# Kernel tuning notes

Hardware: AMD Instinct MI355X
Metric: run time of the kernel (lower is better)

## Reference

```python
import jax, jax.numpy as jnp
import numpy as np

N_NODES = 50000
N_EDGES = 800000
D = 64
B = 64
HL = 128  # lstm hidden
OUT = 32


def setup_inputs() -> dict:
    key = jax.random.key(0)
    ks = jax.random.split(key, 16)
    s = 0.05
    return {
        "x": jax.random.normal(ks[0], (N_NODES, D), jnp.float32),
        "edge_index": jax.random.randint(ks[1], (2, N_EDGES), 0, N_NODES),
        "batch": jnp.sort(jax.random.randint(ks[2], (N_NODES,), 0, B)),
        "w1": jax.random.normal(ks[3], (D, D), jnp.float32) * s,
        "b1": jnp.zeros((D,), jnp.float32),
        "w2": jax.random.normal(ks[4], (D, D), jnp.float32) * s,
        "b2": jnp.zeros((D,), jnp.float32),
        "w3": jax.random.normal(ks[5], (D, D), jnp.float32) * s,
        "b3": jnp.zeros((D,), jnp.float32),
        "w4": jax.random.normal(ks[6], (D, D), jnp.float32) * s,
        "b4": jnp.zeros((D,), jnp.float32),
        "w_ih": jax.random.normal(ks[7], (4 * HL, D), jnp.float32) * s,
        "w_hh": jax.random.normal(ks[8], (4 * HL, HL), jnp.float32) * s,
        "b_ih": jnp.zeros((4 * HL,), jnp.float32),
        "b_hh": jnp.zeros((4 * HL,), jnp.float32),
        "fc_w": jax.random.normal(ks[9], (OUT, HL), jnp.float32) * s,
        "fc_b": jnp.zeros((OUT,), jnp.float32),
        "h0": jax.random.normal(ks[10], (1, B, HL), jnp.float32),
        "c0": jax.random.normal(ks[11], (1, B, HL), jnp.float32),
    }


def _gin(x, edge_index, wA, bA, wB, bB):
    # GINConv with eps=0: MLP(x + sum_{j->i} x_j); scatter-add over edges
    agg = jax.ops.segment_sum(x[edge_index[0]], edge_index[1], num_segments=N_NODES)
    h = x + agg
    h = jax.nn.relu(h @ wA.T + bA)
    return h @ wB.T + bB


def reference(x, edge_index, batch, w1, b1, w2, b2, w3, b3, w4, b4,
              w_ih, w_hh, b_ih, b_hh, fc_w, fc_b, h0, c0):
    h = jax.nn.relu(_gin(x, edge_index, w1, b1, w2, b2))  # dropout = identity (eval)
    h = jax.nn.relu(_gin(h, edge_index, w3, b3, w4, b4))
    # global_mean_pool over graphs
    sums = jax.ops.segment_sum(h, batch, num_segments=B)              # [B, D]
    cnts = jax.ops.segment_sum(jnp.ones((N_NODES,), h.dtype), batch, num_segments=B)
    pooled = sums / jnp.maximum(cnts, 1.0)[:, None]
    # single-step LSTM (PyTorch gate order: i, f, g, o)
    gates = pooled @ w_ih.T + b_ih + h0[0] @ w_hh.T + b_hh            # [B, 4H]
    i, f, g, o = jnp.split(gates, 4, axis=-1)
    c1 = jax.nn.sigmoid(f) * c0[0] + jax.nn.sigmoid(i) * jnp.tanh(g)
    h1 = jax.nn.sigmoid(o) * jnp.tanh(c1)
    logits = h1 @ fc_w.T + fc_b
    probs = jax.nn.softmax(logits, axis=1)
    return probs, h1[None], c1[None]
```

## Files before the change

### kernel.cpp

```cpp
#include <hip/hip_runtime.h>
#include <hip/hip_bf16.h>

#define N_NODES 50000
#define N_EDGES 800000
#define D 64
#define B 64
#define HL 128
#define OUT 32

#define CAP 64
#define STP 72
#define ZROW N_NODES

#define BINS 196
#define EPB 2048
#define LCAP 48
#define BCAP 4608

#define AB 391
#define CB 3125
#define MB 782

typedef __attribute__((ext_vector_type(8))) short          short8;
typedef __attribute__((ext_vector_type(8))) unsigned short ushort8_t;
typedef __attribute__((ext_vector_type(4))) float          floatx4;

__device__ __forceinline__ unsigned short f2bf(float f)
{
    unsigned u = __float_as_uint(f);
    u = (u + 0x7FFFu + ((u >> 16) & 1u)) >> 16;
    return (unsigned short)u;
}
__device__ __forceinline__ float bfLO(unsigned u) { return __uint_as_float(u << 16); }
__device__ __forceinline__ float bfHI(unsigned u) { return __uint_as_float(u & 0xffff0000u); }

__global__ __launch_bounds__(256) void pro_kernel(
    const int*   __restrict__ ei,
    int*         __restrict__ bincnt,
    unsigned*    __restrict__ binbuf,
    const float* __restrict__ x, unsigned short* __restrict__ xb,
    const float* __restrict__ w1, const float* __restrict__ w2,
    const float* __restrict__ w3, const float* __restrict__ w4,
    unsigned short* __restrict__ wb,
    unsigned short* __restrict__ h1,
    float*       __restrict__ psum,
    float*       __restrict__ cnts)
{
    __shared__ int      lcnt[BINS];
    __shared__ int      gbase[BINS];
    __shared__ unsigned lbuf[BINS * LCAP];

    int t = threadIdx.x;

    if (blockIdx.x < AB) {
        if (t < BINS) lcnt[t] = 0;
        __syncthreads();

        int base = blockIdx.x * EPB;
#pragma unroll
        for (int i = 0; i < EPB / 256; ++i) {
            int e = base + i * 256 + t;
            if (e < N_EDGES) {
                int s = ei[e];
                int d = ei[N_EDGES + e];
                int bin = d >> 8;
                unsigned pk = (unsigned)s | ((unsigned)(d & 255) << 16);
                int p = atomicAdd(&lcnt[bin], 1);
                if (p < LCAP) {
                    lbuf[bin * LCAP + p] = pk;
                } else {
                    int q = atomicAdd(&bincnt[bin], 1);
                    if (q < BCAP) binbuf[bin * BCAP + q] = pk;
                }
            }
        }
        __syncthreads();

        if (t < BINS) {
            int m = lcnt[t]; m = (m < LCAP) ? m : LCAP;
            gbase[t] = (m > 0) ? atomicAdd(&bincnt[t], m) : 0;
        }
        __syncthreads();

        int wv = t >> 6, lane = t & 63;
        for (int b = wv; b < BINS; b += 4) {
            int m = lcnt[b]; m = (m < LCAP) ? m : LCAP;
            int gb = gbase[b];
            for (int j = lane; j < m; j += 64)
                if (gb + j < BCAP) binbuf[b * BCAP + gb + j] = lbuf[b * LCAP + j];
        }
    } else if (blockIdx.x < AB + CB) {
        int cb = blockIdx.x - AB;
        int i = cb * 256 + t;
        const float4 v = reinterpret_cast<const float4*>(x)[i];
        ushort4 o;
        o.x = f2bf(v.x); o.y = f2bf(v.y); o.z = f2bf(v.z); o.w = f2bf(v.w);
        reinterpret_cast<ushort4*>(xb)[i] = o;

        if (cb < 64) {
            int j = cb * 256 + t;
            int m = j >> 12, off = j & 4095;
            const float* src = (m == 0) ? w1 : (m == 1) ? w2 : (m == 2) ? w3 : w4;
            wb[j] = f2bf(src[off]);
        }
    } else {
        if (t < D) {
            xb[(size_t)ZROW * D + t] = 0;
            h1[(size_t)ZROW * D + t] = 0;
        }
#pragma unroll
        for (int k = 0; k < 16; ++k)
            psum[t * 16 + k] = 0.0f;
        if (t < B) cnts[t] = 0.0f;
    }
}

__device__ __forceinline__ void build_bucket64(
    const int*      __restrict__ bincnt,
    const unsigned* __restrict__ binbuf,
    unsigned short* lbkt,
    int*            lc,
    int bn0, int t)
{
    {
        ushort8_t fill = {ZROW, ZROW, ZROW, ZROW, ZROW, ZROW, ZROW, ZROW};
        for (int i = t; i < (64 * CAP + 16) / 8; i += 512)
            reinterpret_cast<ushort8_t*>(lbkt)[i] = fill;
    }
    if (t < 64) lc[t] = 0;
    __syncthreads();

    const int bin = bn0 >> 8;
    const int q   = (bn0 >> 6) & 3;
    int m = bincnt[bin]; m = (m < BCAP) ? m : BCAP;
    const unsigned* src = binbuf + bin * BCAP;
    for (int j = t; j < m; j += 512) {
        unsigned pk = src[j];
        int dlow = (pk >> 16) & 255;
        if ((dlow >> 6) == q) {
            int r = dlow & 63;
            int p = atomicAdd(&lc[r], 1);
            if (p < CAP) lbkt[r * CAP + p] = (unsigned short)(pk & 0xFFFFu);
        }
    }
    __syncthreads();
}

__device__ __forceinline__ void gather8_bf16(
    const unsigned short* __restrict__ feat,
    const unsigned short* lbkt,
    const int*            lc,
    unsigned short*       stbase,
    int bn0, int wv, int lane)
{
    const int g = lane >> 4;
    const int c = lane & 15;

#pragma unroll
    for (int b = 0; b < 2; ++b) {
        const int rloc = wv * 8 + b * 4 + g;
        const int node = bn0 + rloc;
        int deg = lc[rloc];
        deg = (deg < CAP) ? deg : CAP;
        int m = (deg + 7) >> 3;
        {
            int t1 = __shfl_xor(m, 16); m = (t1 > m) ? t1 : m;
            int t2 = __shfl_xor(m, 32); m = (t2 > m) ? t2 : m;
        }

        const unsigned short* bkt = lbkt + rloc * CAP;

        uint2 u = *reinterpret_cast<const uint2*>(feat + (size_t)node * D + 4 * c);
        float a0 = bfLO(u.x), a1 = bfHI(u.x);
        float a2 = bfLO(u.y), a3 = bfHI(u.y);

        ushort8_t idx = *reinterpret_cast<const ushort8_t*>(bkt);
        for (int r = 0; r < m; ++r) {
            ushort8_t nxt = *reinterpret_cast<const ushort8_t*>(bkt + (r + 1) * 8);
#pragma unroll
            for (int j = 0; j < 8; ++j) {
                uint2 v = *reinterpret_cast<const uint2*>(
                    feat + (size_t)idx[j] * D + 4 * c);
                a0 += bfLO(v.x); a1 += bfHI(v.x);
                a2 += bfLO(v.y); a3 += bfHI(v.y);
            }
            idx = nxt;
        }

        const int tile = wv >> 1;
        const int row  = (wv & 1) * 8 + b * 4 + g;
        uint2 o;
        o.x = (unsigned)f2bf(a0) | ((unsigned)f2bf(a1) << 16);
        o.y = (unsigned)f2bf(a2) | ((unsigned)f2bf(a3) << 16);
        *reinterpret_cast<uint2*>(stbase + (tile * 16 + row) * STP + 4 * c) = o;
    }
}

__global__ __launch_bounds__(512) void gmlp_kernel(
    const unsigned short* __restrict__ feat,
    const int*            __restrict__ bincnt,
    const unsigned*       __restrict__ binbuf,
    const unsigned short* __restrict__ wAb,
    const float*          __restrict__ bA,
    const unsigned short* __restrict__ wBb,
    const float*          __restrict__ bB,
    unsigned short*       __restrict__ outp)
{
    __shared__ int lc[64];
    __shared__ __align__(16) unsigned short lbkt[64 * CAP + 16];
    __shared__ __align__(16) unsigned short st[4][16 * STP];

    const int t    = threadIdx.x;
    const int wv   = t >> 6;
    const int lane = t & 63;
    const int quad = lane >> 4;
    const int col  = lane & 15;

    const int bn0 = blockIdx.x * 64;

    build_bucket64(bincnt, binbuf, lbkt, lc, bn0, t);

    if (bn0 + wv * 8 < N_NODES)
        gather8_bf16(feat, lbkt, lc, &st[0][0], bn0, wv, lane);
    __syncthreads();

    if (wv >= 4) return;
    const int n0 = bn0 + wv * 16;
    if (n0 >= N_NODES) return;

    float bAl[4], bBl[4];
#pragma unroll
    for (int tt = 0; tt < 4; ++tt) {
        bAl[tt] = bA[tt * 16 + col];
        bBl[tt] = bB[tt * 16 + col];
    }

    short8 WA[4][2], WB[4][2];
#pragma unroll
    for (int tt = 0; tt < 4; ++tt)
#pragma unroll
        for (int k = 0; k < 2; ++k) {
            WA[tt][k] = *reinterpret_cast<const short8*>(
                wAb + (tt * 16 + col) * D + k * 32 + quad * 8);
            WB[tt][k] = *reinterpret_cast<const short8*>(
                wBb + (tt * 16 + col) * D + k * 32 + quad * 8);
        }

    unsigned short* stw = &st[wv][0];

    short8 A0 = *reinterpret_cast<const short8*>(stw + col * STP + 0 * 32 + quad * 8);
    short8 A1 = *reinterpret_cast<const short8*>(stw + col * STP + 1 * 32 + quad * 8);

#pragma unroll
    for (int tt = 0; tt < 4; ++tt) {
        floatx4 c = {0.0f, 0.0f, 0.0f, 0.0f};
        c = __builtin_amdgcn_mfma_f32_16x16x32_bf16(A0, WA[tt][0], c, 0, 0, 0);
        c = __builtin_amdgcn_mfma_f32_16x16x32_bf16(A1, WA[tt][1], c, 0, 0, 0);
#pragma unroll
        for (int r = 0; r < 4; ++r) {
            float v = fmaxf(c[r] + bAl[tt], 0.0f);
            stw[(quad * 4 + r) * STP + tt * 16 + col] = f2bf(v);
        }
    }

    short8 T0 = *reinterpret_cast<const short8*>(stw + col * STP + 0 * 32 + quad * 8);
    short8 T1 = *reinterpret_cast<const short8*>(stw + col * STP + 1 * 32 + quad * 8);

#pragma unroll
    for (int tt = 0; tt < 4; ++tt) {
        floatx4 c = {0.0f, 0.0f, 0.0f, 0.0f};
        c = __builtin_amdgcn_mfma_f32_16x16x32_bf16(T0, WB[tt][0], c, 0, 0, 0);
        c = __builtin_amdgcn_mfma_f32_16x16x32_bf16(T1, WB[tt][1], c, 0, 0, 0);
#pragma unroll
        for (int r = 0; r < 4; ++r) {
            float v = fmaxf(c[r] + bBl[tt], 0.0f);
            outp[(size_t)(n0 + quad * 4 + r) * D + tt * 16 + col] = f2bf(v);
        }
    }
}

__global__ __launch_bounds__(512) void g2mlp_pool_kernel(
    const unsigned short* __restrict__ feat,
    const int*            __restrict__ bincnt,
    const unsigned*       __restrict__ binbuf,
    const unsigned short* __restrict__ wAb,
    const float*          __restrict__ bA,
    const unsigned short* __restrict__ wBb,
    const float*          __restrict__ bB,
    const int*            __restrict__ batch,
    float*                __restrict__ psum,
    float*                __restrict__ cnts)
{
    __shared__ int lc[64];
    __shared__ __align__(16) unsigned short lbkt[64 * CAP + 16];
    __shared__ __align__(16) unsigned short st[4][16 * STP];
    __shared__ float pt[64][D + 1];
    __shared__ int   sbatch[64];

    const int t    = threadIdx.x;
    const int wv   = t >> 6;
    const int lane = t & 63;
    const int quad = lane >> 4;
    const int col  = lane & 15;

    const int bn0 = blockIdx.x * 64;

    if (t < 64) {
        int n = bn0 + t;
        sbatch[t] = (n < N_NODES) ? batch[n] : -1;
    }

    build_bucket64(bincnt, binbuf, lbkt, lc, bn0, t);

    if (bn0 + wv * 8 < N_NODES)
        gather8_bf16(feat, lbkt, lc, &st[0][0], bn0, wv, lane);
    __syncthreads();

    if (wv < 4) {
        const int n0 = bn0 + wv * 16;
        if (n0 < N_NODES) {
            float bAl[4], bBl[4];
#pragma unroll
            for (int tt = 0; tt < 4; ++tt) {
                bAl[tt] = bA[tt * 16 + col];
                bBl[tt] = bB[tt * 16 + col];
            }

            short8 WA[4][2], WB[4][2];
#pragma unroll
            for (int tt = 0; tt < 4; ++tt)
#pragma unroll
                for (int k = 0; k < 2; ++k) {
                    WA[tt][k] = *reinterpret_cast<const short8*>(
                        wAb + (tt * 16 + col) * D + k * 32 + quad * 8);
                    WB[tt][k] = *reinterpret_cast<const short8*>(
                        wBb + (tt * 16 + col) * D + k * 32 + quad * 8);
                }

            unsigned short* stw = &st[wv][0];

            short8 A0 = *reinterpret_cast<const short8*>(stw + col * STP + 0 * 32 + quad * 8);
            short8 A1 = *reinterpret_cast<const short8*>(stw + col * STP + 1 * 32 + quad * 8);

#pragma unroll
            for (int tt = 0; tt < 4; ++tt) {
                floatx4 c = {0.0f, 0.0f, 0.0f, 0.0f};
                c = __builtin_amdgcn_mfma_f32_16x16x32_bf16(A0, WA[tt][0], c, 0, 0, 0);
                c = __builtin_amdgcn_mfma_f32_16x16x32_bf16(A1, WA[tt][1], c, 0, 0, 0);
#pragma unroll
                for (int r = 0; r < 4; ++r) {
                    float v = fmaxf(c[r] + bAl[tt], 0.0f);
                    stw[(quad * 4 + r) * STP + tt * 16 + col] = f2bf(v);
                }
            }

            short8 T0 = *reinterpret_cast<const short8*>(stw + col * STP + 0 * 32 + quad * 8);
            short8 T1 = *reinterpret_cast<const short8*>(stw + col * STP + 1 * 32 + quad * 8);

#pragma unroll
            for (int tt = 0; tt < 4; ++tt) {
                floatx4 c = {0.0f, 0.0f, 0.0f, 0.0f};
                c = __builtin_amdgcn_mfma_f32_16x16x32_bf16(T0, WB[tt][0], c, 0, 0, 0);
                c = __builtin_amdgcn_mfma_f32_16x16x32_bf16(T1, WB[tt][1], c, 0, 0, 0);
#pragma unroll
                for (int r = 0; r < 4; ++r) {
                    float v = fmaxf(c[r] + bBl[tt], 0.0f);
                    pt[wv * 16 + quad * 4 + r][tt * 16 + col] = v;
                }
            }
        } else {
            for (int c2 = 0; c2 < 4; ++c2)
#pragma unroll
                for (int r = 0; r < 4; ++r)
                    pt[wv * 16 + quad * 4 + r][c2 * 16 + col] = 0.0f;
        }
    }
    __syncthreads();

    if (t < 256) {
        int q = t >> 6;
        int d = t & 63;
        float acc = 0.0f;
        int   len = 0;
        int curg = sbatch[q * 16];
#pragma unroll
        for (int r = 0; r < 16; ++r) {
            int row = q * 16 + r;
            int g2 = sbatch[row];
            float v = pt[row][d];
            if (g2 != curg) {
                if (curg >= 0) {
                    atomicAdd(&psum[curg * D + d], acc);
                    if (d == 0) atomicAdd(&cnts[curg], (float)len);
                }
                acc = 0.0f; len = 0;
                curg = g2;
            }
            acc += v;
            len += 1;
        }
        if (curg >= 0) {
            atomicAdd(&psum[curg * D + d], acc);
            if (d == 0) atomicAdd(&cnts[curg], (float)len);
        }
    }
}

__device__ __forceinline__ float sigmoidf_(float x) { return 1.0f / (1.0f + expf(-x)); }

__global__ __launch_bounds__(512) void head_kernel(
    const float* __restrict__ psum,
    const float* __restrict__ cnts,
    const float* __restrict__ w_ih,
    const float* __restrict__ w_hh,
    const float* __restrict__ b_ih,
    const float* __restrict__ b_hh,
    const float* __restrict__ fc_w,
    const float* __restrict__ fc_b,
    const float* __restrict__ h0,
    const float* __restrict__ c0,
    float*       __restrict__ out_probs,
    float*       __restrict__ out_h1,
    float*       __restrict__ out_c1)
{
    int b = blockIdx.x;
    int j = threadIdx.x;

    __shared__ float sp[D];
    __shared__ float sh[HL];
    __shared__ float gates[4 * HL];
    __shared__ float sh1[HL];
    __shared__ float slog[OUT];

    if (j < D) {
        sp[j] = psum[b * D + j] / fmaxf(cnts[b], 1.0f);
    } else if (j < D + HL) {
        sh[j - D] = h0[b * HL + (j - D)];
    }
    __syncthreads();

    {
        float acc = b_ih[j] + b_hh[j];
#pragma unroll
        for (int k = 0; k < D; ++k)  acc = fmaf(sp[k], w_ih[j * D + k], acc);
#pragma unroll
        for (int k = 0; k < HL; ++k) acc = fmaf(sh[k], w_hh[j * HL + k], acc);
        gates[j] = acc;
    }
    __syncthreads();

    if (j < HL) {
        float ig = gates[j];
        float fg = gates[HL + j];
        float gg = gates[2 * HL + j];
        float og = gates[3 * HL + j];
        float c  = sigmoidf_(fg) * c0[b * HL + j] + sigmoidf_(ig) * tanhf(gg);
        float hv = sigmoidf_(og) * tanhf(c);
        out_c1[b * HL + j] = c;
        out_h1[b * HL + j] = hv;
        sh1[j] = hv;
    }
    __syncthreads();

    if (j < OUT) {
        float a = fc_b[j];
#pragma unroll
        for (int k = 0; k < HL; ++k) a = fmaf(sh1[k], fc_w[j * HL + k], a);
        slog[j] = a;
    }
    __syncthreads();

    if (j < OUT) {
        float m = -1e30f;
#pragma unroll
        for (int k = 0; k < OUT; ++k) m = fmaxf(m, slog[k]);
        float s = 0.0f;
#pragma unroll
        for (int k = 0; k < OUT; ++k) s += expf(slog[k] - m);
        out_probs[b * OUT + j] = expf(slog[j] - m) / s;
    }
}

extern "C" void kernel_launch(void* const* d_in, const int* in_sizes, int n_in,
                              void* d_out, int out_size, void* d_ws, size_t ws_size,
                              hipStream_t stream)
{
    const float* x     = (const float*)d_in[0];
    const int*   ei    = (const int*)  d_in[1];
    const int*   batch = (const int*)  d_in[2];
    const float* w1    = (const float*)d_in[3];
    const float* b1    = (const float*)d_in[4];
    const float* w2    = (const float*)d_in[5];
    const float* b2    = (const float*)d_in[6];
    const float* w3    = (const float*)d_in[7];
    const float* b3    = (const float*)d_in[8];
    const float* w4    = (const float*)d_in[9];
    const float* b4    = (const float*)d_in[10];
    const float* w_ih  = (const float*)d_in[11];
    const float* w_hh  = (const float*)d_in[12];
    const float* b_ih  = (const float*)d_in[13];
    const float* b_hh  = (const float*)d_in[14];
    const float* fc_w  = (const float*)d_in[15];
    const float* fc_b  = (const float*)d_in[16];
    const float* h0    = (const float*)d_in[17];
    const float* c0    = (const float*)d_in[18];

    const size_t NR = (size_t)N_NODES + 16;
    int* bincnt = (int*)d_ws;
    unsigned* binbuf = (unsigned*)(bincnt + 256);
    unsigned short* xb = (unsigned short*)(binbuf + (size_t)BINS * BCAP);
    unsigned short* h1 = xb + NR * D;
    unsigned short* wb = h1 + NR * D;
    float* psum = (float*)(wb + 4 * D * D);
    float* cnts = psum + B * D;

    float* out_probs = (float*)d_out;
    float* out_h1    = out_probs + B * OUT;
    float* out_c1    = out_h1 + B * HL;

    hipMemsetAsync(bincnt, 0, 256 * sizeof(int), stream);
    pro_kernel<<<AB + CB + 1, 256, 0, stream>>>(
        ei, bincnt, binbuf, x, xb, w1, w2, w3, w4, wb, h1, psum, cnts);

    gmlp_kernel<<<MB, 512, 0, stream>>>(xb, bincnt, binbuf,
                                        wb, b1, wb + 4096, b2, h1);

    g2mlp_pool_kernel<<<MB, 512, 0, stream>>>(h1, bincnt, binbuf,
                                              wb + 8192, b3, wb + 12288, b4,
                                              batch, psum, cnts);

    head_kernel<<<B, 512, 0, stream>>>(psum, cnts, w_ih, w_hh, b_ih, b_hh,
                                       fc_w, fc_b, h0, c0,
                                       out_probs, out_h1, out_c1);
}
```

Measured before the change: 209.4 us.

## Shrink GIN MLP blocks to 256 threads, swizzle block order, fuse gather per wave

Both GIN aggregate+MLP kernels now run with 256 threads per block. Each of the four waves gathers its own 16 rows into its private staging tile and then runs the MFMA MLP on them, which removes the block-wide barrier between gather and compute and stops half the waves from sitting idle during the MLP. The grid is padded to 800 blocks and remapped with a deswizzle function so that neighbouring node blocks land on the same XCD, aiming for better L2 locality on the bin buffers and feature rows. The trade-offs are twice the gather work per thread and fewer threads to hide gather latency, and the remap assumes a particular round-robin of blocks across XCDs.

```diff
diff --git a/kernel.cpp b/kernel.cpp
--- a/kernel.cpp
+++ b/kernel.cpp
@@ -20,6 +20,7 @@
 #define AB 391
 #define CB 3125
 #define MB 782
+#define SWGRID 800
 
 typedef __attribute__((ext_vector_type(8))) short          short8;
 typedef __attribute__((ext_vector_type(8))) unsigned short ushort8_t;
@@ -33,6 +34,12 @@
 }
 __device__ __forceinline__ float bfLO(unsigned u) { return __uint_as_float(u << 16); }
 __device__ __forceinline__ float bfHI(unsigned u) { return __uint_as_float(u & 0xffff0000u); }
+
+__device__ __forceinline__ int deswizzle_block(int l)
+{
+    int g = ((l >> 5) << 3) | (l & 7);
+    return (g << 2) | ((l >> 3) & 3);
+}
 
 __global__ __launch_bounds__(256) void pro_kernel(
     const int*   __restrict__ ei,
@@ -124,8 +131,8 @@
 {
     {
         ushort8_t fill = {ZROW, ZROW, ZROW, ZROW, ZROW, ZROW, ZROW, ZROW};
-        for (int i = t; i < (64 * CAP + 16) / 8; i += 512)
-            reinterpret_cast<ushort8_t*>(lbkt)[i] = fill;
+        reinterpret_cast<ushort8_t*>(lbkt)[t]       = fill;
+        reinterpret_cast<ushort8_t*>(lbkt)[t + 256] = fill;
     }
     if (t < 64) lc[t] = 0;
     __syncthreads();
@@ -134,7 +141,7 @@
     const int q   = (bn0 >> 6) & 3;
     int m = bincnt[bin]; m = (m < BCAP) ? m : BCAP;
     const unsigned* src = binbuf + bin * BCAP;
-    for (int j = t; j < m; j += 512) {
+    for (int j = t; j < m; j += 256) {
         unsigned pk = src[j];
         int dlow = (pk >> 16) & 255;
         if ((dlow >> 6) == q) {
@@ -146,19 +153,19 @@
     __syncthreads();
 }
 
-__device__ __forceinline__ void gather8_bf16(
+__device__ __forceinline__ void gather16_bf16(
     const unsigned short* __restrict__ feat,
     const unsigned short* lbkt,
     const int*            lc,
-    unsigned short*       stbase,
+    unsigned short*       stw,
     int bn0, int wv, int lane)
 {
     const int g = lane >> 4;
     const int c = lane & 15;
 
 #pragma unroll
-    for (int b = 0; b < 2; ++b) {
-        const int rloc = wv * 8 + b * 4 + g;
+    for (int b = 0; b < 4; ++b) {
+        const int rloc = wv * 16 + b * 4 + g;
         const int node = bn0 + rloc;
         int deg = lc[rloc];
         deg = (deg < CAP) ? deg : CAP;
@@ -187,16 +194,14 @@
             idx = nxt;
         }
 
-        const int tile = wv >> 1;
-        const int row  = (wv & 1) * 8 + b * 4 + g;
         uint2 o;
         o.x = (unsigned)f2bf(a0) | ((unsigned)f2bf(a1) << 16);
         o.y = (unsigned)f2bf(a2) | ((unsigned)f2bf(a3) << 16);
-        *reinterpret_cast<uint2*>(stbase + (tile * 16 + row) * STP + 4 * c) = o;
-    }
-}
-
-__global__ __launch_bounds__(512) void gmlp_kernel(
+        *reinterpret_cast<uint2*>(stw + (b * 4 + g) * STP + 4 * c) = o;
+    }
+}
+
+__global__ __launch_bounds__(256) void gmlp_kernel(
     const unsigned short* __restrict__ feat,
     const int*            __restrict__ bincnt,
     const unsigned*       __restrict__ binbuf,
@@ -210,22 +215,20 @@
     __shared__ __align__(16) unsigned short lbkt[64 * CAP + 16];
     __shared__ __align__(16) unsigned short st[4][16 * STP];
 
+    const int o = deswizzle_block(blockIdx.x);
+    if (o >= MB) return;
+
     const int t    = threadIdx.x;
     const int wv   = t >> 6;
     const int lane = t & 63;
     const int quad = lane >> 4;
     const int col  = lane & 15;
 
-    const int bn0 = blockIdx.x * 64;
+    const int bn0 = o * 64;
+    const int n0  = bn0 + wv * 16;
 
     build_bucket64(bincnt, binbuf, lbkt, lc, bn0, t);
 
-    if (bn0 + wv * 8 < N_NODES)
-        gather8_bf16(feat, lbkt, lc, &st[0][0], bn0, wv, lane);
-    __syncthreads();
-
-    if (wv >= 4) return;
-    const int n0 = bn0 + wv * 16;
     if (n0 >= N_NODES) return;
 
     float bAl[4], bBl[4];
@@ -248,6 +251,8 @@
 
     unsigned short* stw = &st[wv][0];
 
+    gather16_bf16(feat, lbkt, lc, stw, bn0, wv, lane);
+
     short8 A0 = *reinterpret_cast<const short8*>(stw + col * STP + 0 * 32 + quad * 8);
     short8 A1 = *reinterpret_cast<const short8*>(stw + col * STP + 1 * 32 + quad * 8);
 
@@ -279,7 +284,7 @@
     }
 }
 
-__global__ __launch_bounds__(512) void g2mlp_pool_kernel(
+__global__ __launch_bounds__(256) void g2mlp_pool_kernel(
     const unsigned short* __restrict__ feat,
     const int*            __restrict__ bincnt,
     const unsigned*       __restrict__ binbuf,
@@ -297,13 +302,18 @@
     __shared__ float pt[64][D + 1];
     __shared__ int   sbatch[64];
 
+    const int o = deswizzle_block(blockIdx.x);
+    if (o >= MB) return;
+
     const int t    = threadIdx.x;
     const int wv   = t >> 6;
     const int lane = t & 63;
     const int quad = lane >> 4;
     const int col  = lane & 15;
 
-    const int bn0 = blockIdx.x * 64;
+    const int bn0 = o * 64;
+    const int n0  = bn0 + wv * 16;
+    const bool active = (n0 < N_NODES);
 
     if (t < 64) {
         int n = bn0 + t;
@@ -312,97 +322,90 @@
 
     build_bucket64(bincnt, binbuf, lbkt, lc, bn0, t);
 
-    if (bn0 + wv * 8 < N_NODES)
-        gather8_bf16(feat, lbkt, lc, &st[0][0], bn0, wv, lane);
-    __syncthreads();
-
-    if (wv < 4) {
-        const int n0 = bn0 + wv * 16;
-        if (n0 < N_NODES) {
-            float bAl[4], bBl[4];
-#pragma unroll
-            for (int tt = 0; tt < 4; ++tt) {
-                bAl[tt] = bA[tt * 16 + col];
-                bBl[tt] = bB[tt * 16 + col];
+    if (active) {
+        float bAl[4], bBl[4];
+#pragma unroll
+        for (int tt = 0; tt < 4; ++tt) {
+            bAl[tt] = bA[tt * 16 + col];
+            bBl[tt] = bB[tt * 16 + col];
+        }
+
+        short8 WA[4][2], WB[4][2];
+#pragma unroll
+        for (int tt = 0; tt < 4; ++tt)
+#pragma unroll
+            for (int k = 0; k < 2; ++k) {
+                WA[tt][k] = *reinterpret_cast<const short8*>(
+                    wAb + (tt * 16 + col) * D + k * 32 + quad * 8);
+                WB[tt][k] = *reinterpret_cast<const short8*>(
+                    wBb + (tt * 16 + col) * D + k * 32 + quad * 8);
             }
 
-            short8 WA[4][2], WB[4][2];
-#pragma unroll
-            for (int tt = 0; tt < 4; ++tt)
-#pragma unroll
-                for (int k = 0; k < 2; ++k) {
-                    WA[tt][k] = *reinterpret_cast<const short8*>(
-                        wAb + (tt * 16 + col) * D + k * 32 + quad * 8);
-                    WB[tt][k] = *reinterpret_cast<const short8*>(
-                        wBb + (tt * 16 + col) * D + k * 32 + quad * 8);
-                }
-
-            unsigned short* stw = &st[wv][0];
-
-            short8 A0 = *reinterpret_cast<const short8*>(stw + col * STP + 0 * 32 + quad * 8);
-            short8 A1 = *reinterpret_cast<const short8*>(stw + col * STP + 1 * 32 + quad * 8);
-
-#pragma unroll
-            for (int tt = 0; tt < 4; ++tt) {
-                floatx4 c = {0.0f, 0.0f, 0.0f, 0.0f};
-                c = __builtin_amdgcn_mfma_f32_16x16x32_bf16(A0, WA[tt][0], c, 0, 0, 0);
-                c = __builtin_amdgcn_mfma_f32_16x16x32_bf16(A1, WA[tt][1], c, 0, 0, 0);
-#pragma unroll
-                for (int r = 0; r < 4; ++r) {
-                    float v = fmaxf(c[r] + bAl[tt], 0.0f);
-                    stw[(quad * 4 + r) * STP + tt * 16 + col] = f2bf(v);
-                }
+        unsigned short* stw = &st[wv][0];
+
+        gather16_bf16(feat, lbkt, lc, stw, bn0, wv, lane);
+
+        short8 A0 = *reinterpret_cast<const short8*>(stw + col * STP + 0 * 32 + quad * 8);
+        short8 A1 = *reinterpret_cast<const short8*>(stw + col * STP + 1 * 32 + quad * 8);
+
+#pragma unroll
+        for (int tt = 0; tt < 4; ++tt) {
+            floatx4 c = {0.0f, 0.0f, 0.0f, 0.0f};
+            c = __builtin_amdgcn_mfma_f32_16x16x32_bf16(A0, WA[tt][0], c, 0, 0, 0);
+            c = __builtin_amdgcn_mfma_f32_16x16x32_bf16(A1, WA[tt][1], c, 0, 0, 0);
+#pragma unroll
+            for (int r = 0; r < 4; ++r) {
+                float v = fmaxf(c[r] + bAl[tt], 0.0f);
+                stw[(quad * 4 + r) * STP + tt * 16 + col] = f2bf(v);
             }
-
-            short8 T0 = *reinterpret_cast<const short8*>(stw + col * STP + 0 * 32 + quad * 8);
-            short8 T1 = *reinterpret_cast<const short8*>(stw + col * STP + 1 * 32 + quad * 8);
-
-#pragma unroll
-            for (int tt = 0; tt < 4; ++tt) {
-                floatx4 c = {0.0f, 0.0f, 0.0f, 0.0f};
-                c = __builtin_amdgcn_mfma_f32_16x16x32_bf16(T0, WB[tt][0], c, 0, 0, 0);
-                c = __builtin_amdgcn_mfma_f32_16x16x32_bf16(T1, WB[tt][1], c, 0, 0, 0);
-#pragma unroll
-                for (int r = 0; r < 4; ++r) {
-                    float v = fmaxf(c[r] + bBl[tt], 0.0f);
-                    pt[wv * 16 + quad * 4 + r][tt * 16 + col] = v;
-                }
+        }
+
+        short8 T0 = *reinterpret_cast<const short8*>(stw + col * STP + 0 * 32 + quad * 8);
+        short8 T1 = *reinterpret_cast<const short8*>(stw + col * STP + 1 * 32 + quad * 8);
+
+#pragma unroll
+        for (int tt = 0; tt < 4; ++tt) {
+            floatx4 c = {0.0f, 0.0f, 0.0f, 0.0f};
+            c = __builtin_amdgcn_mfma_f32_16x16x32_bf16(T0, WB[tt][0], c, 0, 0, 0);
+            c = __builtin_amdgcn_mfma_f32_16x16x32_bf16(T1, WB[tt][1], c, 0, 0, 0);
+#pragma unroll
+            for (int r = 0; r < 4; ++r) {
+                float v = fmaxf(c[r] + bBl[tt], 0.0f);
+                pt[wv * 16 + quad * 4 + r][tt * 16 + col] = v;
             }
-        } else {
-            for (int c2 = 0; c2 < 4; ++c2)
-#pragma unroll
-                for (int r = 0; r < 4; ++r)
-                    pt[wv * 16 + quad * 4 + r][c2 * 16 + col] = 0.0f;
-        }
-    }
-    __syncthreads();
-
-    if (t < 256) {
-        int q = t >> 6;
-        int d = t & 63;
-        float acc = 0.0f;
-        int   len = 0;
-        int curg = sbatch[q * 16];
-#pragma unroll
-        for (int r = 0; r < 16; ++r) {
-            int row = q * 16 + r;
-            int g2 = sbatch[row];
-            float v = pt[row][d];
-            if (g2 != curg) {
-                if (curg >= 0) {
-                    atomicAdd(&psum[curg * D + d], acc);
-                    if (d == 0) atomicAdd(&cnts[curg], (float)len);
-                }
-                acc = 0.0f; len = 0;
-                curg = g2;
+        }
+    } else {
+        for (int c2 = 0; c2 < 4; ++c2)
+#pragma unroll
+            for (int r = 0; r < 4; ++r)
+                pt[wv * 16 + quad * 4 + r][c2 * 16 + col] = 0.0f;
+    }
+    __syncthreads();
+
+    int q = t >> 6;
+    int d = t & 63;
+    float acc = 0.0f;
+    int   len = 0;
+    int curg = sbatch[q * 16];
+#pragma unroll
+    for (int r = 0; r < 16; ++r) {
+        int row = q * 16 + r;
+        int g2 = sbatch[row];
+        float v = pt[row][d];
+        if (g2 != curg) {
+            if (curg >= 0) {
+                atomicAdd(&psum[curg * D + d], acc);
+                if (d == 0) atomicAdd(&cnts[curg], (float)len);
             }
-            acc += v;
-            len += 1;
-        }
-        if (curg >= 0) {
-            atomicAdd(&psum[curg * D + d], acc);
-            if (d == 0) atomicAdd(&cnts[curg], (float)len);
-        }
+            acc = 0.0f; len = 0;
+            curg = g2;
+        }
+        acc += v;
+        len += 1;
+    }
+    if (curg >= 0) {
+        atomicAdd(&psum[curg * D + d], acc);
+        if (d == 0) atomicAdd(&cnts[curg], (float)len);
     }
 }
 
@@ -522,12 +525,12 @@
     pro_kernel<<<AB + CB + 1, 256, 0, stream>>>(
         ei, bincnt, binbuf, x, xb, w1, w2, w3, w4, wb, h1, psum, cnts);
 
-    gmlp_kernel<<<MB, 512, 0, stream>>>(xb, bincnt, binbuf,
-                                        wb, b1, wb + 4096, b2, h1);
-
-    g2mlp_pool_kernel<<<MB, 512, 0, stream>>>(h1, bincnt, binbuf,
-                                              wb + 8192, b3, wb + 12288, b4,
-                                              batch, psum, cnts);
+    gmlp_kernel<<<SWGRID, 256, 0, stream>>>(xb, bincnt, binbuf,
+                                            wb, b1, wb + 4096, b2, h1);
+
+    g2mlp_pool_kernel<<<SWGRID, 256, 0, stream>>>(h1, bincnt, binbuf,
+                                                  wb + 8192, b3, wb + 12288, b4,
+                                                  batch, psum, cnts);
 
     head_kernel<<<B, 512, 0, stream>>>(psum, cnts, w_ih, w_hh, b_ih, b_hh,
                                        fc_w, fc_b, h0, c0,
```

New measurement: 208.3 us. No clear change (-0.5%).
